# Performance work log

Measured on AMD Instinct MI355X. Metric: run time of the kernel, lower is better.

The kernel has to match this reference:

```python
import jax, jax.numpy as jnp
import numpy as np

B, N, K = 16, 512, 30
H = 128
NHEADS = 4
NLAYERS = 3
VOCAB = 20
NUM_RBF = 16
NUM_POS = 16
NEG_INF = jnp.float32(np.finfo(np.float32).min)


def _ln(x, eps=1e-6):
    m = jnp.mean(x, -1, keepdims=True)
    v = jnp.var(x, -1, keepdims=True)
    return (x - m) / jnp.sqrt(v + eps)


def _gather_nodes(nodes, E_idx):
    # nodes [B,N,C], E_idx [B,N,K] -> [B,N,K,C]
    return jax.vmap(lambda n, idx: n[idx])(nodes, E_idx)


def _normalize(x):
    return x / (jnp.linalg.norm(x, axis=-1, keepdims=True) + 1e-7)


def _dihedrals(X):
    b, n = X.shape[0], X.shape[1]
    Xb = X[:, :, :3, :].reshape(b, 3 * n, 3)  # N, CA, C atoms flattened
    dX = Xb[:, 1:] - Xb[:, :-1]
    U = _normalize(dX)
    u2, u1, u0 = U[:, :-2], U[:, 1:-1], U[:, 2:]
    n2 = _normalize(jnp.cross(u2, u1))
    n1 = _normalize(jnp.cross(u1, u0))
    cosD = jnp.clip(jnp.sum(n2 * n1, -1), -1.0 + 1e-7, 1.0 - 1e-7)
    Dang = jnp.sign(jnp.sum(u2 * n1, -1)) * jnp.arccos(cosD)
    Dang = jnp.pad(Dang, ((0, 0), (1, 2)))
    Dang = Dang.reshape(b, n, 3)
    return jnp.concatenate([jnp.cos(Dang), jnp.sin(Dang)], -1)  # [B,N,6]


def _features(X, mask, Wfn, bfn, Wfe, bfe):
    X_ca = X[:, :, 1, :]
    mask2d = mask[:, :, None] * mask[:, None, :]
    dX = X_ca[:, :, None, :] - X_ca[:, None, :, :]
    D = mask2d * jnp.sqrt(jnp.sum(dX * dX, -1) + 1e-6)  # [B,N,N]
    D_max = jnp.max(D, -1, keepdims=True)
    D_adjust = D + (1.0 - mask2d) * D_max
    negD, E_idx = jax.lax.top_k(-D_adjust, K)  # K nearest neighbors
    D_neighbors = -negD
    mu = jnp.linspace(0.0, 20.0, NUM_RBF)
    sigma = 20.0 / NUM_RBF
    rbf = jnp.exp(-(((D_neighbors[..., None] - mu) / sigma) ** 2))  # [B,N,K,16]
    ii = jnp.arange(N)[None, :, None]
    d = (E_idx - ii)[..., None].astype(jnp.float32)
    freq = jnp.exp(jnp.arange(0, NUM_POS, 2, dtype=jnp.float32) * (-np.log(10000.0) / NUM_POS))
    ang = d * freq
    epos = jnp.concatenate([jnp.cos(ang), jnp.sin(ang)], -1)  # [B,N,K,16]
    E = jnp.concatenate([epos, rbf], -1)  # [B,N,K,32]
    V = _dihedrals(X)
    V = _ln(V @ Wfn + bfn)
    E = _ln(E @ Wfe + bfe)
    return V, E, E_idx


def _attn(hV, hE, WQ, WK, WV, WO, mask_attend=None):
    b, n, h = hV.shape
    k = hE.shape[2]
    d = h // NHEADS
    Q = (hV @ WQ).reshape(b, n, NHEADS, d)
    Kt = (hE @ WK).reshape(b, n, k, NHEADS, d)
    Vt = (hE @ WV).reshape(b, n, k, NHEADS, d)
    logits = jnp.einsum('bnhd,bnkhd->bnhk', Q, Kt) / np.sqrt(d).astype(np.float32)
    if mask_attend is not None:
        m = mask_attend[:, :, None, :]
        logits = jnp.where(m > 0, logits, NEG_INF)
        attend = jax.nn.softmax(logits, -1) * m
    else:
        attend = jax.nn.softmax(logits, -1)
    out = jnp.einsum('bnhk,bnkhd->bnhd', attend, Vt).reshape(b, n, h)
    return out @ WO


def _layer(hV, hEV, WQ, WK, WV, WO, W1, b1, W2, b2, mask_V=None, mask_attend=None):
    dh = _attn(hV, hEV, WQ, WK, WV, WO, mask_attend)
    hV = _ln(hV + dh)
    dh = jax.nn.relu(hV @ W1 + b1) @ W2 + b2
    hV = _ln(hV + dh)
    if mask_V is not None:
        hV = mask_V[..., None] * hV
    return hV


def _forward(X, mask, S, Wfn, bfn, Wfe, bfe, Wv, bv, We, be, Ws,
             enc_WQ, enc_WK, enc_WV, enc_WO, enc_W1, enc_b1, enc_W2, enc_b2,
             dec_WQ, dec_WK, dec_WV, dec_WO, dec_W1, dec_b1, dec_W2, dec_b2,
             W_out, b_out):
    V, E, E_idx = _features(X, mask, Wfn, bfn, Wfe, bfe)
    h_V = V @ Wv + bv
    h_E = E @ We + be
    # encoder attention mask
    mask_nb = _gather_nodes(mask[..., None], E_idx)[..., 0]
    mask_attend_enc = mask[:, :, None] * mask_nb
    for l in range(NLAYERS):
        h_EV = jnp.concatenate([h_E, _gather_nodes(h_V, E_idx)], -1)
        h_V = _layer(h_V, h_EV, enc_WQ[l], enc_WK[l], enc_WV[l], enc_WO[l],
                     enc_W1[l], enc_b1[l], enc_W2[l], enc_b2[l],
                     mask_V=mask, mask_attend=mask_attend_enc)
    # decoder: identity permutation -> rank == position, ar mask = E_idx < i
    ar = (E_idx < jnp.arange(N)[None, :, None]).astype(h_V.dtype)
    mask_attend = ar[..., None]  # [B,N,K,1]
    h_S = Ws[S]
    h_ES = jnp.concatenate([h_E, _gather_nodes(h_S, E_idx)], -1)
    h_ES_enc = jnp.concatenate([h_E, jnp.zeros_like(h_E[..., :H])], -1)
    h_ESV_enc = jnp.concatenate([h_ES_enc, _gather_nodes(h_V, E_idx)], -1)
    mask_1D = mask[:, :, None, None]
    mask_bw = mask_1D * mask_attend
    mask_fw = mask_1D * (1.0 - mask_attend)
    h_fw = mask_fw * h_ESV_enc
    for l in range(NLAYERS):
        h_ESV = jnp.concatenate([h_ES, _gather_nodes(h_V, E_idx)], -1)
        h_ESV = mask_bw * h_ESV + h_fw
        h_V = _layer(h_V, h_ESV, dec_WQ[l], dec_WK[l], dec_WV[l], dec_WO[l],
                     dec_W1[l], dec_b1[l], dec_W2[l], dec_b2[l], mask_V=mask)
    logits = h_V @ W_out + b_out
    return jax.nn.log_softmax(logits, -1)


def setup_inputs():
    key = jax.random.key(0)
    ks = iter(jax.random.split(key, 80))

    def lin(i, o):
        return jax.random.normal(next(ks), (i, o), dtype=jnp.float32) * (1.0 / np.sqrt(i)).astype(np.float32)

    def stack(i, o):
        return jnp.stack([lin(i, o) for _ in range(NLAYERS)])

    inp = {}
    inp['X'] = jax.random.normal(next(ks), (B, N, 4, 3), dtype=jnp.float32) * 3.0
    inp['mask'] = jnp.ones((B, N), jnp.float32)
    inp['S'] = jax.random.randint(next(ks), (B, N), 0, VOCAB)
    inp['Wfn'] = lin(6, H); inp['bfn'] = jnp.zeros((H,), jnp.float32)
    inp['Wfe'] = lin(NUM_POS + NUM_RBF, H); inp['bfe'] = jnp.zeros((H,), jnp.float32)
    inp['Wv'] = lin(H, H); inp['bv'] = jnp.zeros((H,), jnp.float32)
    inp['We'] = lin(H, H); inp['be'] = jnp.zeros((H,), jnp.float32)
    inp['Ws'] = jax.random.normal(next(ks), (VOCAB, H), dtype=jnp.float32) * 0.1
    inp['enc_WQ'] = stack(H, H); inp['enc_WK'] = stack(2 * H, H)
    inp['enc_WV'] = stack(2 * H, H); inp['enc_WO'] = stack(H, H)
    inp['enc_W1'] = stack(H, 4 * H); inp['enc_b1'] = jnp.zeros((NLAYERS, 4 * H), jnp.float32)
    inp['enc_W2'] = stack(4 * H, H); inp['enc_b2'] = jnp.zeros((NLAYERS, H), jnp.float32)
    inp['dec_WQ'] = stack(H, H); inp['dec_WK'] = stack(3 * H, H)
    inp['dec_WV'] = stack(3 * H, H); inp['dec_WO'] = stack(H, H)
    inp['dec_W1'] = stack(H, 4 * H); inp['dec_b1'] = jnp.zeros((NLAYERS, 4 * H), jnp.float32)
    inp['dec_W2'] = stack(4 * H, H); inp['dec_b2'] = jnp.zeros((NLAYERS, H), jnp.float32)
    inp['W_out'] = lin(H, VOCAB); inp['b_out'] = jnp.zeros((VOCAB,), jnp.float32)
    return inp


def reference(X, mask, S, Wfn, bfn, Wfe, bfe, Wv, bv, We, be, Ws,
              enc_WQ, enc_WK, enc_WV, enc_WO, enc_W1, enc_b1, enc_W2, enc_b2,
              dec_WQ, dec_WK, dec_WV, dec_WO, dec_W1, dec_b1, dec_W2, dec_b2,
              W_out, b_out):
    return _forward(X, mask, S, Wfn, bfn, Wfe, bfe, Wv, bv, We, be, Ws,
                    enc_WQ, enc_WK, enc_WV, enc_WO, enc_W1, enc_b1, enc_W2, enc_b2,
                    dec_WQ, dec_WK, dec_WV, dec_WO, dec_W1, dec_b1, dec_W2, dec_b2,
                    W_out, b_out)
```

## Files before the change

### kernel.cpp

```cpp
#include <hip/hip_runtime.h>
#include <hip/hip_bf16.h>
#include <math.h>

#define DEVFN __device__ __forceinline__

constexpr int B_ = 16, N_ = 512, K_ = 30, H_ = 128;
constexpr int NH_ = 4, V_ = 20;
constexpr int BN_ = B_ * N_;
constexpr float NEG_INF_ = -3.4028235e38f;
constexpr int FRAG_ = H_ * H_;
constexpr int FRAG2_ = H_ * 4 * H_;

typedef unsigned short ushort_t;
using short8 = __attribute__((ext_vector_type(8))) short;
using f32x4  = __attribute__((ext_vector_type(4))) float;

DEVFN ushort_t bf16rn(float x) {
  unsigned u = __float_as_uint(x);
  return (ushort_t)((u + 0x7fffu + ((u >> 16) & 1u)) >> 16);
}
DEVFN float bf16tof(ushort_t h) { return __uint_as_float(((unsigned)h) << 16); }

__global__ __launch_bounds__(256) void topk_kernel(const float* __restrict__ X,
    const float* __restrict__ mask, int* __restrict__ E_idx, float* __restrict__ Dnb) {
  __shared__ float xs[N_ * 3];
  __shared__ float ds[N_];
  __shared__ float fred[4];
  __shared__ unsigned long long kred[4];
  int b = blockIdx.x / N_, i = blockIdx.x % N_;
  int t = threadIdx.x;
  for (int j = t; j < N_; j += 256) {
    const float* p = X + ((size_t)(b * N_ + j) * 4 + 1) * 3;
    xs[j * 3 + 0] = p[0]; xs[j * 3 + 1] = p[1]; xs[j * 3 + 2] = p[2];
  }
  __syncthreads();
  float xi0 = xs[i * 3], xi1 = xs[i * 3 + 1], xi2 = xs[i * 3 + 2];
  float mi = mask[b * N_ + i];
  float lmax = -3.4e38f;
  for (int j = t; j < N_; j += 256) {
    float dx = __fsub_rn(xi0, xs[j * 3]);
    float dy = __fsub_rn(xi1, xs[j * 3 + 1]);
    float dz = __fsub_rn(xi2, xs[j * 3 + 2]);
    float m2 = __fmul_rn(mi, mask[b * N_ + j]);
    float s = __fadd_rn(__fadd_rn(__fadd_rn(__fmul_rn(dx, dx), __fmul_rn(dy, dy)),
                                  __fmul_rn(dz, dz)), 1e-6f);
    float D = __fmul_rn(m2, __fsqrt_rn(s));
    ds[j] = D;
    lmax = fmaxf(lmax, D);
  }
  #pragma unroll
  for (int off = 32; off > 0; off >>= 1) lmax = fmaxf(lmax, __shfl_xor(lmax, off, 64));
  if ((t & 63) == 0) fred[t >> 6] = lmax;
  __syncthreads();
  float Dmax = fmaxf(fmaxf(fred[0], fred[1]), fmaxf(fred[2], fred[3]));
  for (int j = t; j < N_; j += 256) {
    float m2 = __fmul_rn(mi, mask[b * N_ + j]);
    ds[j] = __fadd_rn(ds[j], __fmul_rn(__fsub_rn(1.f, m2), Dmax));
  }
  __syncthreads();
  for (int kk = 0; kk < K_; kk++) {
    unsigned long long best = ~0ull;
    for (int j = t; j < N_; j += 256) {
      unsigned long long key = (((unsigned long long)__float_as_uint(ds[j])) << 32)
                             | (unsigned)(N_ - 1 - j);
      if (key < best) best = key;
    }
    #pragma unroll
    for (int off = 32; off > 0; off >>= 1) {
      unsigned long long o = __shfl_xor(best, off, 64);
      if (o < best) best = o;
    }
    if ((t & 63) == 0) kred[t >> 6] = best;
    __syncthreads();
    if (t == 0) {
      unsigned long long k0 = kred[0];
      #pragma unroll
      for (int q = 1; q < 4; q++) if (kred[q] < k0) k0 = kred[q];
      int j = N_ - 1 - (int)(k0 & 0xffffffffull);
      E_idx[blockIdx.x * K_ + kk] = j;
      Dnb[blockIdx.x * K_ + kk] = __uint_as_float((unsigned)(k0 >> 32));
      ds[j] = 3.4028235e38f;
    }
    __syncthreads();
  }
}

DEVFN void load_atom(const float* X, int b, int m, float* p) {
  const float* q = X + ((size_t)(b * N_ + m / 3) * 4 + (m % 3)) * 3;
  p[0] = q[0]; p[1] = q[1]; p[2] = q[2];
}
DEVFN void cross3(const float* a, const float* b, float* c) {
  c[0] = a[1] * b[2] - a[2] * b[1];
  c[1] = a[2] * b[0] - a[0] * b[2];
  c[2] = a[0] * b[1] - a[1] * b[0];
}
DEVFN void norm3(float* v) {
  float n = sqrtf(v[0] * v[0] + v[1] * v[1] + v[2] * v[2]) + 1e-7f;
  v[0] /= n; v[1] /= n; v[2] /= n;
}
__global__ __launch_bounds__(256) void dihedral_kernel(const float* __restrict__ X, float* __restrict__ Vf) {
  int idx = blockIdx.x * blockDim.x + threadIdx.x;
  if (idx >= BN_) return;
  int b = idx / N_, n = idx % N_;
  float cs[3], sn[3];
  for (int s = 0; s < 3; s++) {
    int p = 3 * n + s;
    float a = 0.f;
    if (p >= 1 && p <= 3 * N_ - 3) {
      int tt = p - 1;
      float u[3][3], prev[3], cur[3];
      load_atom(X, b, tt, prev);
      for (int q = 0; q < 3; q++) {
        load_atom(X, b, tt + q + 1, cur);
        float d0 = cur[0] - prev[0], d1 = cur[1] - prev[1], d2 = cur[2] - prev[2];
        float nr = sqrtf(d0 * d0 + d1 * d1 + d2 * d2) + 1e-7f;
        u[q][0] = d0 / nr; u[q][1] = d1 / nr; u[q][2] = d2 / nr;
        prev[0] = cur[0]; prev[1] = cur[1]; prev[2] = cur[2];
      }
      float n2v[3], n1v[3];
      cross3(u[0], u[1], n2v); norm3(n2v);
      cross3(u[1], u[2], n1v); norm3(n1v);
      float cd = n2v[0] * n1v[0] + n2v[1] * n1v[1] + n2v[2] * n1v[2];
      cd = fminf(fmaxf(cd, -1.f + 1e-7f), 1.f - 1e-7f);
      float dt = u[0][0] * n1v[0] + u[0][1] * n1v[1] + u[0][2] * n1v[2];
      float sg = (dt > 0.f) ? 1.f : ((dt < 0.f) ? -1.f : 0.f);
      a = sg * acosf(cd);
    }
    cs[s] = cosf(a); sn[s] = sinf(a);
  }
  float* o = Vf + (size_t)idx * 6;
  o[0] = cs[0]; o[1] = cs[1]; o[2] = cs[2]; o[3] = sn[0]; o[4] = sn[1]; o[5] = sn[2];
}

__global__ __launch_bounds__(H_) void node_embed_kernel(const float* __restrict__ Vf,
    const float* __restrict__ Wfn, const float* __restrict__ bfn,
    const float* __restrict__ Wv, const float* __restrict__ bv, float* __restrict__ hV) {
  int node = blockIdx.x, t = threadIdx.x;
  const int w = t >> 6, l = t & 63;
  __shared__ float v6[6];
  __shared__ __attribute__((aligned(16))) float t1[H_];
  __shared__ float wred[2];
  if (t < 6) v6[t] = Vf[(size_t)node * 6 + t];
  __syncthreads();
  float acc = bfn[t];
  for (int f = 0; f < 6; f++) acc = fmaf(v6[f], Wfn[f * H_ + t], acc);
  float s1 = acc;
  #pragma unroll
  for (int off = 32; off > 0; off >>= 1) s1 += __shfl_xor(s1, off, 64);
  if (l == 0) wred[w] = s1;
  __syncthreads();
  float mean = (wred[0] + wred[1]) * (1.f / H_);
  float d0 = acc - mean;
  float s2 = d0 * d0;
  #pragma unroll
  for (int off = 32; off > 0; off >>= 1) s2 += __shfl_xor(s2, off, 64);
  __syncthreads();
  if (l == 0) wred[w] = s2;
  __syncthreads();
  float var = (wred[0] + wred[1]) * (1.f / H_);
  t1[t] = d0 * rsqrtf(var + 1e-6f);
  __syncthreads();
  float o = bv[t];
  for (int j4 = 0; j4 < H_ / 4; j4++) {
    float4 xv = ((const float4*)t1)[j4];
    int j = j4 * 4;
    o = fmaf(xv.x, Wv[(j + 0) * H_ + t],
        fmaf(xv.y, Wv[(j + 1) * H_ + t],
        fmaf(xv.z, Wv[(j + 2) * H_ + t],
        fmaf(xv.w, Wv[(j + 3) * H_ + t], o))));
  }
  hV[(size_t)node * H_ + t] = o;
}

__global__ __launch_bounds__(256) void prep_edge_w_kernel(const float* __restrict__ Wfe,
    const float* __restrict__ We, ushort_t* __restrict__ feHi, ushort_t* __restrict__ feLo,
    ushort_t* __restrict__ weHi, ushort_t* __restrict__ weLo) {
  if (blockIdx.x == 0) {
    for (int i = 0; i < 4096 / 256; i++) {
      int lin = i * 256 + threadIdx.x;
      int k = lin >> 7, c = lin & 127;
      float x = Wfe[lin];
      int gk = k >> 3, j = k & 7;
      int nt = c >> 4, cc = c & 15;
      int oidx = (nt * 64 + gk * 16 + cc) * 8 + j;
      ushort_t hb = bf16rn(x);
      feHi[oidx] = hb;
      feLo[oidx] = bf16rn(x - bf16tof(hb));
    }
  } else {
    for (int i = 0; i < FRAG_ / 256; i++) {
      int lin = i * 256 + threadIdx.x;
      int k = lin >> 7, c = lin & 127;
      float x = We[lin];
      int ks = k >> 5, gk = (k >> 3) & 3, j = k & 7;
      int nt = c >> 4, cc = c & 15;
      int oidx = ((ks * 8 + nt) * 64 + gk * 16 + cc) * 8 + j;
      ushort_t hb = bf16rn(x);
      weHi[oidx] = hb;
      weLo[oidx] = bf16rn(x - bf16tof(hb));
    }
  }
}

__global__ __launch_bounds__(256) void prep_wkt_kernel(const float* __restrict__ eWK,
    const float* __restrict__ dWK, float* __restrict__ outT) {
  int m = blockIdx.x;
  const float* W = (m < 3) ? (eWK + (size_t)m * 2 * H_ * H_)
                           : (dWK + (size_t)(m - 3) * 3 * H_ * H_);
  float* o = outT + (size_t)m * FRAG_;
  for (int i = 0; i < FRAG_ / 256; i++) {
    int lin = i * 256 + threadIdx.x;
    int c = lin >> 7, f = lin & 127;
    o[lin] = W[f * H_ + c];
  }
}

constexpr int EEB_ = 32;
constexpr int FPS_ = 40;
__global__ __launch_bounds__(128) void edge_embed_kernel(const int* __restrict__ E_idx,
    const float* __restrict__ Dnb,
    const ushort_t* __restrict__ feHi, const ushort_t* __restrict__ feLo,
    const float* __restrict__ bfe,
    const ushort_t* __restrict__ weHi, const ushort_t* __restrict__ weLo,
    const float* __restrict__ be, float* __restrict__ hE) {
  int e0 = blockIdx.x * EEB_, t = threadIdx.x;
  const int w = t >> 6, l = t & 63, c0 = l & 15, g = l >> 4;
  __shared__ ushort_t fhi[EEB_ * FPS_], flo[EEB_ * FPS_];
  __shared__ __attribute__((aligned(16))) char sbuf[EEB_ * H_ * 4];
  float* buf = (float*)sbuf;
  ushort_t* p2hi = (ushort_t*)sbuf;
  ushort_t* p2lo = (ushort_t*)(sbuf + EEB_ * H_ * 2);
  __shared__ float mst[EEB_], ist[EEB_];

  #pragma unroll
  for (int it = 0; it < 8; it++) {
    int id = it * 128 + t;
    int r = id >> 5, f = id & 31;
    int e = e0 + r;
    int n = (e / K_) % N_;
    float v;
    if (f < 16) {
      int jj = (f < 8) ? f : (f - 8);
      float freq = expf(-logf(10000.f) * (2.f * jj) / 16.f);
      float ang = (float)(E_idx[e] - n) * freq;
      v = (f < 8) ? cosf(ang) : sinf(ang);
    } else {
      int rr = f - 16;
      float mu = 20.f * (float)rr / 15.f;
      float z = (Dnb[e] - mu) * (1.f / 1.25f);
      v = expf(-z * z);
    }
    ushort_t hb = bf16rn(v);
    fhi[r * FPS_ + f] = hb;
    flo[r * FPS_ + f] = bf16rn(v - bf16tof(hb));
  }
  __syncthreads();

  {
    short8 ah[2], al[2];
    #pragma unroll
    for (int mt = 0; mt < 2; mt++) {
      int r = mt * 16 + c0;
      ah[mt] = *(const short8*)&fhi[r * FPS_ + g * 8];
      al[mt] = *(const short8*)&flo[r * FPS_ + g * 8];
    }
    #pragma unroll
    for (int nt = 0; nt < 4; nt++) {
      int ntg = w * 4 + nt;
      size_t boff = (size_t)((ntg * 64 + l) * 8);
      short8 bh = *(const short8*)(feHi + boff);
      short8 bl = *(const short8*)(feLo + boff);
      int c = ntg * 16 + c0;
      float bb = bfe[c];
      #pragma unroll
      for (int mt = 0; mt < 2; mt++) {
        f32x4 a = f32x4{0.f, 0.f, 0.f, 0.f};
        a = __builtin_amdgcn_mfma_f32_16x16x32_bf16(ah[mt], bh, a, 0, 0, 0);
        a = __builtin_amdgcn_mfma_f32_16x16x32_bf16(al[mt], bh, a, 0, 0, 0);
        a = __builtin_amdgcn_mfma_f32_16x16x32_bf16(ah[mt], bl, a, 0, 0, 0);
        a = __builtin_amdgcn_mfma_f32_16x16x32_bf16(al[mt], bl, a, 0, 0, 0);
        #pragma unroll
        for (int j = 0; j < 4; j++) {
          int row = mt * 16 + g * 4 + j;
          buf[row * H_ + c] = a[j] + bb;
        }
      }
    }
  }
  __syncthreads();

  {
    int row = t >> 2, li = t & 3;
    float s = 0.f;
    for (int i = 0; i < 32; i++) {
      int col = li + 4 * ((i + row) & 31);
      s += buf[row * H_ + col];
    }
    s += __shfl_xor(s, 1, 64); s += __shfl_xor(s, 2, 64);
    float mean = s * (1.f / H_);
    float vs = 0.f;
    for (int i = 0; i < 32; i++) {
      int col = li + 4 * ((i + row) & 31);
      float d = buf[row * H_ + col] - mean;
      vs = fmaf(d, d, vs);
    }
    vs += __shfl_xor(vs, 1, 64); vs += __shfl_xor(vs, 2, 64);
    if (li == 0) { mst[row] = mean; ist[row] = rsqrtf(vs * (1.f / H_) + 1e-6f); }
  }
  __syncthreads();

  float vreg[32];
  #pragma unroll
  for (int it = 0; it < 4; it++) {
    int id = it * 128 + t;
    int r = id >> 4, u = id & 15;
    float mean = mst[r], inv = ist[r];
    #pragma unroll
    for (int e2 = 0; e2 < 8; e2++) vreg[it * 8 + e2] = (buf[r * H_ + u * 8 + e2] - mean) * inv;
  }
  __syncthreads();
  #pragma unroll
  for (int it = 0; it < 4; it++) {
    int id = it * 128 + t;
    int r = id >> 4, u = id & 15;
    short8 h8, l8;
    #pragma unroll
    for (int e2 = 0; e2 < 8; e2++) {
      float x = vreg[it * 8 + e2];
      ushort_t hb = bf16rn(x);
      h8[e2] = (short)hb;
      l8[e2] = (short)bf16rn(x - bf16tof(hb));
    }
    int us = u ^ (r & 15);
    *(short8*)&p2hi[r * 128 + us * 8] = h8;
    *(short8*)&p2lo[r * 128 + us * 8] = l8;
  }
  __syncthreads();

  short8 ah2[2][4], al2[2][4];
  #pragma unroll
  for (int mt = 0; mt < 2; mt++) {
    int r = mt * 16 + c0;
    #pragma unroll
    for (int ks = 0; ks < 4; ks++) {
      int us = (ks * 4 + g) ^ c0;
      ah2[mt][ks] = *(const short8*)&p2hi[r * 128 + us * 8];
      al2[mt][ks] = *(const short8*)&p2lo[r * 128 + us * 8];
    }
  }
  f32x4 acc2[2][4];
  #pragma unroll
  for (int mt = 0; mt < 2; mt++)
    #pragma unroll
    for (int nt = 0; nt < 4; nt++) acc2[mt][nt] = f32x4{0.f, 0.f, 0.f, 0.f};
  #pragma unroll
  for (int ks = 0; ks < 4; ks++) {
    #pragma unroll
    for (int nt = 0; nt < 4; nt++) {
      int ntg = w * 4 + nt;
      size_t boff = (size_t)(((ks * 8 + ntg) * 64 + l) * 8);
      short8 bh = *(const short8*)(weHi + boff);
      short8 bl = *(const short8*)(weLo + boff);
      #pragma unroll
      for (int mt = 0; mt < 2; mt++) {
        acc2[mt][nt] = __builtin_amdgcn_mfma_f32_16x16x32_bf16(ah2[mt][ks], bh, acc2[mt][nt], 0, 0, 0);
        acc2[mt][nt] = __builtin_amdgcn_mfma_f32_16x16x32_bf16(al2[mt][ks], bh, acc2[mt][nt], 0, 0, 0);
        acc2[mt][nt] = __builtin_amdgcn_mfma_f32_16x16x32_bf16(ah2[mt][ks], bl, acc2[mt][nt], 0, 0, 0);
        acc2[mt][nt] = __builtin_amdgcn_mfma_f32_16x16x32_bf16(al2[mt][ks], bl, acc2[mt][nt], 0, 0, 0);
      }
    }
  }
  #pragma unroll
  for (int mt = 0; mt < 2; mt++) {
    #pragma unroll
    for (int nt = 0; nt < 4; nt++) {
      int c = (w * 4 + nt) * 16 + c0;
      float bb = be[c];
      #pragma unroll
      for (int j = 0; j < 4; j++) {
        int row = mt * 16 + g * 4 + j;
        hE[(size_t)(e0 + row) * H_ + c] = acc2[mt][nt][j] + bb;
      }
    }
  }
}

__global__ __launch_bounds__(128) void node_proj_kernel(const float* __restrict__ x1,
    const float* __restrict__ Wa1, const float* __restrict__ Wb1,
    float* __restrict__ oa, float* __restrict__ ob) {
  constexpr int NT = 16;
  int n0 = blockIdx.x * NT, t = threadIdx.x;
  __shared__ __attribute__((aligned(16))) float xs1[NT * H_];
  #pragma unroll
  for (int u = 0; u < NT; u++) xs1[u * H_ + t] = x1[(size_t)(n0 + u) * H_ + t];
  __syncthreads();
  float aa[NT], ab[NT];
  #pragma unroll
  for (int u = 0; u < NT; u++) { aa[u] = 0.f; ab[u] = 0.f; }
  for (int j4 = 0; j4 < H_ / 4; j4++) {
    int j = j4 * 4;
    float wa0 = Wa1[(j + 0) * H_ + t], wa1 = Wa1[(j + 1) * H_ + t];
    float wa2 = Wa1[(j + 2) * H_ + t], wa3 = Wa1[(j + 3) * H_ + t];
    float wb0 = Wb1[(j + 0) * H_ + t], wb1 = Wb1[(j + 1) * H_ + t];
    float wb2 = Wb1[(j + 2) * H_ + t], wb3 = Wb1[(j + 3) * H_ + t];
    #pragma unroll
    for (int u = 0; u < NT; u++) {
      float4 xv = ((const float4*)(xs1 + u * H_))[j4];
      aa[u] = fmaf(xv.x, wa0, fmaf(xv.y, wa1, fmaf(xv.z, wa2, fmaf(xv.w, wa3, aa[u]))));
      ab[u] = fmaf(xv.x, wb0, fmaf(xv.y, wb1, fmaf(xv.z, wb2, fmaf(xv.w, wb3, ab[u]))));
    }
  }
  #pragma unroll
  for (int u = 0; u < NT; u++) {
    oa[(size_t)(n0 + u) * H_ + t] = aa[u];
    ob[(size_t)(n0 + u) * H_ + t] = ab[u];
  }
}

__global__ __launch_bounds__(128) void node_proj3_kernel(const int* __restrict__ S,
    const float* __restrict__ Ws, const float* __restrict__ din, const float* __restrict__ henc,
    const float* __restrict__ WK2, const float* __restrict__ WV2,
    const float* __restrict__ WK3, const float* __restrict__ WV3,
    float* __restrict__ nKb, float* __restrict__ nVb,
    float* __restrict__ nKe, float* __restrict__ nVe) {
  constexpr int NT = 8;
  int n0 = blockIdx.x * NT, t = threadIdx.x;
  __shared__ __attribute__((aligned(16))) float xs1[NT * H_];
  __shared__ __attribute__((aligned(16))) float xs2[NT * H_];
  __shared__ __attribute__((aligned(16))) float xs3[NT * H_];
  #pragma unroll
  for (int u = 0; u < NT; u++) {
    int node = n0 + u;
    xs1[u * H_ + t] = Ws[(size_t)S[node] * H_ + t];
    xs2[u * H_ + t] = din[(size_t)node * H_ + t];
    xs3[u * H_ + t] = henc[(size_t)node * H_ + t];
  }
  __syncthreads();
  float aKb[NT], aVb[NT], aKe[NT], aVe[NT];
  #pragma unroll
  for (int u = 0; u < NT; u++) { aKb[u] = 0.f; aVb[u] = 0.f; aKe[u] = 0.f; aVe[u] = 0.f; }
  for (int j4 = 0; j4 < H_ / 4; j4++) {
    int j = j4 * 4;
    float k20 = WK2[(j + 0) * H_ + t], k21 = WK2[(j + 1) * H_ + t];
    float k22 = WK2[(j + 2) * H_ + t], k23 = WK2[(j + 3) * H_ + t];
    float v20 = WV2[(j + 0) * H_ + t], v21 = WV2[(j + 1) * H_ + t];
    float v22 = WV2[(j + 2) * H_ + t], v23 = WV2[(j + 3) * H_ + t];
    float k30 = WK3[(j + 0) * H_ + t], k31 = WK3[(j + 1) * H_ + t];
    float k32 = WK3[(j + 2) * H_ + t], k33 = WK3[(j + 3) * H_ + t];
    float v30 = WV3[(j + 0) * H_ + t], v31 = WV3[(j + 1) * H_ + t];
    float v32 = WV3[(j + 2) * H_ + t], v33 = WV3[(j + 3) * H_ + t];
    #pragma unroll
    for (int u = 0; u < NT; u++) {
      float4 a = ((const float4*)(xs1 + u * H_))[j4];
      float4 b = ((const float4*)(xs2 + u * H_))[j4];
      float4 c = ((const float4*)(xs3 + u * H_))[j4];
      aKb[u] = fmaf(a.x, k20, fmaf(a.y, k21, fmaf(a.z, k22, fmaf(a.w, k23, aKb[u]))));
      aKb[u] = fmaf(b.x, k30, fmaf(b.y, k31, fmaf(b.z, k32, fmaf(b.w, k33, aKb[u]))));
      aVb[u] = fmaf(a.x, v20, fmaf(a.y, v21, fmaf(a.z, v22, fmaf(a.w, v23, aVb[u]))));
      aVb[u] = fmaf(b.x, v30, fmaf(b.y, v31, fmaf(b.z, v32, fmaf(b.w, v33, aVb[u]))));
      aKe[u] = fmaf(c.x, k30, fmaf(c.y, k31, fmaf(c.z, k32, fmaf(c.w, k33, aKe[u]))));
      aVe[u] = fmaf(c.x, v30, fmaf(c.y, v31, fmaf(c.z, v32, fmaf(c.w, v33, aVe[u]))));
    }
  }
  #pragma unroll
  for (int u = 0; u < NT; u++) {
    size_t g = (size_t)(n0 + u) * H_ + t;
    nKb[g] = aKb[u]; nVb[g] = aVb[u]; nKe[g] = aKe[u]; nVe[g] = aVe[u];
  }
}

__global__ __launch_bounds__(256) void prep_wfrag2_kernel(const float* __restrict__ eW1,
    const float* __restrict__ eW2, const float* __restrict__ dW1, const float* __restrict__ dW2,
    ushort_t* __restrict__ hiOut, ushort_t* __restrict__ loOut) {
  int m = blockIdx.x;
  const float* W; int C;
  if (m < 3)      { W = eW1 + (size_t)m * FRAG2_;       C = 4 * H_; }
  else if (m < 6) { W = eW2 + (size_t)(m - 3) * FRAG2_; C = H_; }
  else if (m < 9) { W = dW1 + (size_t)(m - 6) * FRAG2_; C = 4 * H_; }
  else            { W = dW2 + (size_t)(m - 9) * FRAG2_; C = H_; }
  ushort_t* hi = hiOut + (size_t)m * FRAG2_;
  ushort_t* lo = loOut + (size_t)m * FRAG2_;
  int ntn = C >> 4;
  int cshift = (C == 512) ? 9 : 7;
  for (int i = 0; i < FRAG2_ / 256; i++) {
    int lin = i * 256 + threadIdx.x;
    int k = lin >> cshift, c = lin & (C - 1);
    float x = W[lin];
    int ks = k >> 5, gk = (k >> 3) & 3, j = k & 7;
    int nt = c >> 4, cc = c & 15;
    int lane = gk * 16 + cc;
    int oidx = ((ks * ntn + nt) * 64 + lane) * 8 + j;
    ushort_t hb = bf16rn(x);
    hi[oidx] = hb;
    lo[oidx] = bf16rn(x - bf16tof(hb));
  }
}

template<bool ENC>
__global__ __launch_bounds__(128) void attn_kernel(const float* __restrict__ hV_in,
    const float* __restrict__ hE, const int* __restrict__ E_idx, const float* __restrict__ mask,
    const float* __restrict__ WQ, const float* __restrict__ WK1T, const float* __restrict__ WV1,
    const float* __restrict__ WO,
    const float* __restrict__ nKb, const float* __restrict__ nVb,
    const float* __restrict__ nKe, const float* __restrict__ nVe,
    float* __restrict__ hV_out) {
  const int node = blockIdx.x;
  const int b = node / N_, n = node % N_;
  const int t = threadIdx.x;
  const int w = t >> 6, l = t & 63;
  const int head = t >> 5, lane32 = t & 31;

  __shared__ __attribute__((aligned(16))) float heb[K_ * H_];
  __shared__ float x0s[H_];
  __shared__ float qs[H_];
  __shared__ float qa[4][H_ + 4];
  __shared__ float ob[H_];
  __shared__ float scb[NH_ * 32];
  __shared__ int nbs[K_];
  __shared__ float wred[2];

  x0s[t] = hV_in[(size_t)node * H_ + t];
  if (t < K_) nbs[t] = E_idx[node * K_ + t];
  {
    const float4* src = (const float4*)(hE + (size_t)node * (K_ * H_));
    float4* dst = (float4*)heb;
    #pragma unroll
    for (int i = 0; i < (K_ * H_ / 4) / 128 + 1; i++) {
      int id = i * 128 + t;
      if (id < K_ * H_ / 4) dst[id] = src[id];
    }
  }
  if ((t & 31) >= K_) scb[t] = NEG_INF_;
  __syncthreads();

  float qreg = 0.f;
  for (int j4 = 0; j4 < H_ / 4; j4++) {
    float4 xv = ((const float4*)x0s)[j4];
    int j = j4 * 4;
    qreg = fmaf(xv.x, WQ[(j + 0) * H_ + t],
           fmaf(xv.y, WQ[(j + 1) * H_ + t],
           fmaf(xv.z, WQ[(j + 2) * H_ + t],
           fmaf(xv.w, WQ[(j + 3) * H_ + t], qreg))));
  }
  qs[t] = qreg;
  float mi = mask[b * N_ + n];
  __syncthreads();

  {
    float a0 = 0.f, a1 = 0.f, a2 = 0.f, a3 = 0.f;
    #pragma unroll 4
    for (int c = 0; c < 32; c++) {
      a0 = fmaf(WK1T[(c      ) * H_ + t], qs[c      ], a0);
      a1 = fmaf(WK1T[(c + 32 ) * H_ + t], qs[c + 32 ], a1);
      a2 = fmaf(WK1T[(c + 64 ) * H_ + t], qs[c + 64 ], a2);
      a3 = fmaf(WK1T[(c + 96 ) * H_ + t], qs[c + 96 ], a3);
    }
    qa[0][t] = a0; qa[1][t] = a1; qa[2][t] = a2; qa[3][t] = a3;
  }
  __syncthreads();

  const float qk0 = qa[head][lane32],      qk1 = qa[head][lane32 + 32];
  const float qk2 = qa[head][lane32 + 64], qk3 = qa[head][lane32 + 96];
  constexpr int KT = 10;
  const float scale = 0.17677669529663687f;
  for (int kt = 0; kt < K_; kt += KT) {
    float gb[KT], ge[KT], gm[KT];
    #pragma unroll
    for (int u = 0; u < KT; u++) {
      int nb = nbs[kt + u];
      size_t nbg = (size_t)(b * N_ + nb) * H_ + t;
      gb[u] = nKb[nbg];
      if (!ENC) ge[u] = nKe[nbg];
      else      gm[u] = mask[b * N_ + nb];
    }
    #pragma unroll
    for (int u = 0; u < KT; u++) {
      int k = kt + u;
      int nb = nbs[k];
      const float* he = heb + k * H_;
      float ep = fmaf(qk0, he[lane32],
                 fmaf(qk1, he[lane32 + 32],
                 fmaf(qk2, he[lane32 + 64], qk3 * he[lane32 + 96])));
      float prod;
      if (ENC) {
        prod = fmaf(qreg, gb[u], ep);
      } else {
        float ar = (nb < n) ? 1.f : 0.f;
        float bw = mi * ar, fw = mi * (1.f - ar);
        float nodek = fmaf(bw, gb[u], fw * ge[u]);
        prod = fmaf(mi, ep, qreg * nodek);
      }
      #pragma unroll
      for (int off = 16; off > 0; off >>= 1) prod += __shfl_xor(prod, off, 32);
      if (lane32 == 0) {
        if (ENC) {
          float m2 = mi * gm[u];
          scb[head * 32 + k] = (m2 > 0.f) ? prod * scale : NEG_INF_;
        } else {
          scb[head * 32 + k] = prod * scale;
        }
      }
    }
  }
  __syncthreads();

  {
    float s = scb[t];
    float mx = s;
    #pragma unroll
    for (int off = 16; off > 0; off >>= 1) mx = fmaxf(mx, __shfl_xor(mx, off, 32));
    float ev = expf(s - mx);
    float sum = ev;
    #pragma unroll
    for (int off = 16; off > 0; off >>= 1) sum += __shfl_xor(sum, off, 32);
    scb[t] = ev / sum;
  }
  __syncthreads();

  {
    float a0 = 0.f, a1 = 0.f, a2 = 0.f, a3 = 0.f;
    #pragma unroll
    for (int k = 0; k < K_; k++) {
      float hv = heb[k * H_ + t];
      a0 = fmaf(scb[0 * 32 + k], hv, a0);
      a1 = fmaf(scb[1 * 32 + k], hv, a1);
      a2 = fmaf(scb[2 * 32 + k], hv, a2);
      a3 = fmaf(scb[3 * 32 + k], hv, a3);
    }
    qa[0][t] = a0; qa[1][t] = a1; qa[2][t] = a2; qa[3][t] = a3;
  }
  float onode = 0.f;
  for (int kt = 0; kt < K_; kt += KT) {
    float gv[KT], gve[KT];
    #pragma unroll
    for (int u = 0; u < KT; u++) {
      int nb = nbs[kt + u];
      size_t nbg = (size_t)(b * N_ + nb) * H_ + t;
      gv[u] = nVb[nbg];
      if (!ENC) gve[u] = nVe[nbg];
    }
    #pragma unroll
    for (int u = 0; u < KT; u++) {
      int k = kt + u;
      float att = scb[head * 32 + k];
      if (ENC) {
        onode = fmaf(att, gv[u], onode);
      } else {
        int nb = nbs[k];
        float ar = (nb < n) ? 1.f : 0.f;
        float bw = mi * ar, fw = mi * (1.f - ar);
        onode = fmaf(att, fmaf(bw, gv[u], fw * gve[u]), onode);
      }
    }
  }
  __syncthreads();

  float oe = 0.f;
  {
    const float* agh = qa[head];
    #pragma unroll 4
    for (int f = 0; f < H_; f++) oe = fmaf(agh[f], WV1[f * H_ + t], oe);
  }
  float o = ENC ? (oe + onode) : fmaf(mi, oe, onode);
  ob[t] = o; __syncthreads();

  float dh = 0.f;
  for (int j4 = 0; j4 < H_ / 4; j4++) {
    float4 ov = ((const float4*)ob)[j4];
    int j = j4 * 4;
    dh = fmaf(ov.x, WO[(j + 0) * H_ + t],
         fmaf(ov.y, WO[(j + 1) * H_ + t],
         fmaf(ov.z, WO[(j + 2) * H_ + t],
         fmaf(ov.w, WO[(j + 3) * H_ + t], dh))));
  }
  float r = x0s[t] + dh;
  float s1 = r;
  #pragma unroll
  for (int off = 32; off > 0; off >>= 1) s1 += __shfl_xor(s1, off, 64);
  if (l == 0) wred[w] = s1;
  __syncthreads();
  float mean = (wred[0] + wred[1]) * (1.f / H_);
  float d0 = r - mean;
  float s2 = d0 * d0;
  #pragma unroll
  for (int off = 32; off > 0; off >>= 1) s2 += __shfl_xor(s2, off, 64);
  __syncthreads();
  if (l == 0) wred[w] = s2;
  __syncthreads();
  float var = (wred[0] + wred[1]) * (1.f / H_);
  hV_out[(size_t)node * H_ + t] = d0 * rsqrtf(var + 1e-6f);
}

constexpr int NTF_ = 8;
__global__ __launch_bounds__(128) void ffn_kernel(float* __restrict__ hV, const float* __restrict__ mask,
    const ushort_t* __restrict__ w1hi, const ushort_t* __restrict__ w1lo,
    const ushort_t* __restrict__ w2hi, const ushort_t* __restrict__ w2lo,
    const float* __restrict__ b1, const float* __restrict__ b2) {
  int n0 = blockIdx.x * NTF_, t = threadIdx.x;
  const int w = t >> 6, l = t & 63, c0 = l & 15, g = l >> 4;
  __shared__ __attribute__((aligned(16))) ushort_t xhi[16 * H_], xlo[16 * H_];
  __shared__ __attribute__((aligned(16))) ushort_t hpl[2][2 * 16 * H_];
  __shared__ float mst[16], ist[16];
  float* obuf = (float*)&hpl[0][0];

  #pragma unroll
  for (int it = 0; it < 2; it++) {
    int id = it * 128 + t;
    int r = id >> 4, u = id & 15;
    short8 h8 = {0,0,0,0,0,0,0,0}, l8 = {0,0,0,0,0,0,0,0};
    if (r < NTF_) {
      const float4* p = (const float4*)(hV + (size_t)(n0 + r) * H_ + u * 8);
      float4 f0 = p[0], f1 = p[1];
      float xv[8] = {f0.x, f0.y, f0.z, f0.w, f1.x, f1.y, f1.z, f1.w};
      #pragma unroll
      for (int e = 0; e < 8; e++) {
        ushort_t hb = bf16rn(xv[e]);
        h8[e] = (short)hb;
        l8[e] = (short)bf16rn(xv[e] - bf16tof(hb));
      }
    }
    int us = u ^ (r & 15);
    *(short8*)&xhi[r * 128 + us * 8] = h8;
    *(short8*)&xlo[r * 128 + us * 8] = l8;
  }
  __syncthreads();

  short8 axh[4], axl[4];
  #pragma unroll
  for (int ks = 0; ks < 4; ks++) {
    int us = ((ks * 4 + g) ^ c0) * 8;
    axh[ks] = *(const short8*)&xhi[c0 * 128 + us];
    axl[ks] = *(const short8*)&xlo[c0 * 128 + us];
  }

  ushort_t* myhhi = &hpl[w][0];
  ushort_t* myhlo = &hpl[w][16 * H_];
  f32x4 accO[8];
  #pragma unroll
  for (int nt = 0; nt < 8; nt++) accO[nt] = f32x4{0.f, 0.f, 0.f, 0.f};

  #pragma unroll
  for (int cc = 0; cc < 2; cc++) {
    int c = 2 * w + cc;
    f32x4 a1[8];
    #pragma unroll
    for (int nt = 0; nt < 8; nt++) a1[nt] = f32x4{0.f, 0.f, 0.f, 0.f};
    #pragma unroll
    for (int ks = 0; ks < 4; ks++) {
      #pragma unroll
      for (int nt = 0; nt < 8; nt++) {
        size_t boff = (size_t)(((ks * 32 + (c * 8 + nt)) * 64 + l) * 8);
        short8 bh = *(const short8*)(w1hi + boff);
        short8 bl = *(const short8*)(w1lo + boff);
        a1[nt] = __builtin_amdgcn_mfma_f32_16x16x32_bf16(axh[ks], bh, a1[nt], 0, 0, 0);
        a1[nt] = __builtin_amdgcn_mfma_f32_16x16x32_bf16(axl[ks], bh, a1[nt], 0, 0, 0);
        a1[nt] = __builtin_amdgcn_mfma_f32_16x16x32_bf16(axh[ks], bl, a1[nt], 0, 0, 0);
        a1[nt] = __builtin_amdgcn_mfma_f32_16x16x32_bf16(axl[ks], bl, a1[nt], 0, 0, 0);
      }
    }
    #pragma unroll
    for (int nt = 0; nt < 8; nt++) {
      int col = nt * 16 + c0;
      float bb = b1[c * 128 + col];
      #pragma unroll
      for (int j = 0; j < 4; j++) {
        int row = g * 4 + j;
        float hv = fmaxf(a1[nt][j] + bb, 0.f);
        ushort_t hb = bf16rn(hv);
        ushort_t lb = bf16rn(hv - bf16tof(hb));
        int us2 = ((col >> 3) ^ row) * 8 + (col & 7);
        myhhi[row * 128 + us2] = hb;
        myhlo[row * 128 + us2] = lb;
      }
    }
    #pragma unroll
    for (int ks = 0; ks < 4; ks++) {
      int us2 = ((ks * 4 + g) ^ c0) * 8;
      short8 ahh = *(const short8*)&myhhi[c0 * 128 + us2];
      short8 ahl = *(const short8*)&myhlo[c0 * 128 + us2];
      #pragma unroll
      for (int nt = 0; nt < 8; nt++) {
        size_t boff = (size_t)((((c * 4 + ks) * 8 + nt) * 64 + l) * 8);
        short8 bh = *(const short8*)(w2hi + boff);
        short8 bl = *(const short8*)(w2lo + boff);
        accO[nt] = __builtin_amdgcn_mfma_f32_16x16x32_bf16(ahh, bh, accO[nt], 0, 0, 0);
        accO[nt] = __builtin_amdgcn_mfma_f32_16x16x32_bf16(ahl, bh, accO[nt], 0, 0, 0);
        accO[nt] = __builtin_amdgcn_mfma_f32_16x16x32_bf16(ahh, bl, accO[nt], 0, 0, 0);
        accO[nt] = __builtin_amdgcn_mfma_f32_16x16x32_bf16(ahl, bl, accO[nt], 0, 0, 0);
      }
    }
  }

  if (w == 0) {
    #pragma unroll
    for (int nt = 0; nt < 8; nt++) {
      #pragma unroll
      for (int j = 0; j < 4; j++) {
        int row = g * 4 + j;
        if (row < NTF_) obuf[row * H_ + nt * 16 + c0] = accO[nt][j];
      }
    }
  }
  __syncthreads();
  if (w == 1) {
    #pragma unroll
    for (int nt = 0; nt < 8; nt++) {
      #pragma unroll
      for (int j = 0; j < 4; j++) {
        int row = g * 4 + j;
        if (row < NTF_) obuf[row * H_ + nt * 16 + c0] += accO[nt][j];
      }
    }
  }
  __syncthreads();

  float rv[NTF_];
  {
    int un = t >> 3, e = t & 7;
    float bb = b2[t];
    #pragma unroll
    for (int u = 0; u < NTF_; u++) {
      int us = (un ^ u) * 8 + e;
      float xr = bf16tof(xhi[u * 128 + us]) + bf16tof(xlo[u * 128 + us]);
      rv[u] = xr + obuf[u * H_ + t] + bb;
    }
  }
  #pragma unroll
  for (int u = 0; u < NTF_; u++) obuf[u * H_ + t] = rv[u];
  __syncthreads();
  {
    int row = t >> 3, li = t & 7;
    float s = 0.f;
    if (row < NTF_) {
      for (int i = 0; i < 16; i++) s += obuf[row * H_ + li + 8 * i];
    }
    s += __shfl_xor(s, 1, 64); s += __shfl_xor(s, 2, 64); s += __shfl_xor(s, 4, 64);
    float mean = s * (1.f / H_);
    float vs = 0.f;
    if (row < NTF_) {
      for (int i = 0; i < 16; i++) {
        float d = obuf[row * H_ + li + 8 * i] - mean;
        vs = fmaf(d, d, vs);
      }
    }
    vs += __shfl_xor(vs, 1, 64); vs += __shfl_xor(vs, 2, 64); vs += __shfl_xor(vs, 4, 64);
    if (li == 0 && row < NTF_) { mst[row] = mean; ist[row] = rsqrtf(vs * (1.f / H_) + 1e-6f); }
  }
  __syncthreads();
  #pragma unroll
  for (int u = 0; u < NTF_; u++) {
    float y = (rv[u] - mst[u]) * ist[u] * mask[n0 + u];
    hV[(size_t)(n0 + u) * H_ + t] = y;
  }
}

__global__ __launch_bounds__(128) void out_kernel(const float* __restrict__ hV,
    const float* __restrict__ Wout, const float* __restrict__ bout, float* __restrict__ out) {
  int g = threadIdx.x >> 6, t = threadIdx.x & 63;
  int node = blockIdx.x * 2 + g;
  __shared__ float x[2][H_];
  __shared__ float lg[2][V_];
  __shared__ float lse[2];
  x[g][t] = hV[(size_t)node * H_ + t];
  x[g][t + 64] = hV[(size_t)node * H_ + t + 64];
  __syncthreads();
  if (t < V_) {
    float a = bout[t];
    for (int h = 0; h < H_; h++) a = fmaf(x[g][h], Wout[h * V_ + t], a);
    lg[g][t] = a;
  }
  __syncthreads();
  if (t == 0) {
    float mx = -3.4e38f;
    for (int v = 0; v < V_; v++) mx = fmaxf(mx, lg[g][v]);
    float s = 0.f;
    for (int v = 0; v < V_; v++) s += expf(lg[g][v] - mx);
    lse[g] = mx + logf(s);
  }
  __syncthreads();
  if (t < V_) out[(size_t)node * V_ + t] = lg[g][t] - lse[g];
}

extern "C" void kernel_launch(void* const* d_in, const int* in_sizes, int n_in,
                              void* d_out, int out_size, void* d_ws, size_t ws_size,
                              hipStream_t stream) {
  const float* X    = (const float*)d_in[0];
  const float* mask = (const float*)d_in[1];
  const int*   S    = (const int*)d_in[2];
  const float* Wfn  = (const float*)d_in[3];
  const float* bfn  = (const float*)d_in[4];
  const float* Wfe  = (const float*)d_in[5];
  const float* bfe  = (const float*)d_in[6];
  const float* Wv   = (const float*)d_in[7];
  const float* bv   = (const float*)d_in[8];
  const float* We   = (const float*)d_in[9];
  const float* be   = (const float*)d_in[10];
  const float* Ws   = (const float*)d_in[11];
  const float* eWQ  = (const float*)d_in[12];
  const float* eWK  = (const float*)d_in[13];
  const float* eWV  = (const float*)d_in[14];
  const float* eWO  = (const float*)d_in[15];
  const float* eW1  = (const float*)d_in[16];
  const float* eb1  = (const float*)d_in[17];
  const float* eW2  = (const float*)d_in[18];
  const float* eb2  = (const float*)d_in[19];
  const float* dWQ  = (const float*)d_in[20];
  const float* dWK  = (const float*)d_in[21];
  const float* dWV  = (const float*)d_in[22];
  const float* dWO  = (const float*)d_in[23];
  const float* dW1  = (const float*)d_in[24];
  const float* db1  = (const float*)d_in[25];
  const float* dW2  = (const float*)d_in[26];
  const float* db2  = (const float*)d_in[27];
  const float* Wout = (const float*)d_in[28];
  const float* bout = (const float*)d_in[29];
  float* out = (float*)d_out;

  char* w = (char*)d_ws;
  int*    eidx = (int*)w;     w += (size_t)BN_ * K_ * 4;
  float*  dnb  = (float*)w;   w += (size_t)BN_ * K_ * 4;
  float*  vf   = (float*)w;   w += (size_t)BN_ * 6 * 4;
  float*  hVa  = (float*)w;   w += (size_t)BN_ * H_ * 4;
  float*  hVb  = (float*)w;   w += (size_t)BN_ * H_ * 4;
  float*  hVc  = (float*)w;   w += (size_t)BN_ * H_ * 4;
  float*  nKb  = (float*)w;   w += (size_t)BN_ * H_ * 4;
  float*  nVb  = (float*)w;   w += (size_t)BN_ * H_ * 4;
  float*  nKe  = (float*)w;   w += (size_t)BN_ * H_ * 4;
  float*  nVe  = (float*)w;   w += (size_t)BN_ * H_ * 4;
  float*  hE   = (float*)w;   w += (size_t)BN_ * K_ * H_ * 4;
  float*  wkt  = (float*)w;   w += (size_t)6 * FRAG_ * 4;
  ushort_t* wf2Hi = (ushort_t*)w; w += (size_t)12 * FRAG2_ * 2;
  ushort_t* wf2Lo = (ushort_t*)w; w += (size_t)12 * FRAG2_ * 2;
  ushort_t* feHi = (ushort_t*)w; w += (size_t)4096 * 2;
  ushort_t* feLo = (ushort_t*)w; w += (size_t)4096 * 2;
  ushort_t* weHi = (ushort_t*)w; w += (size_t)FRAG_ * 2;
  ushort_t* weLo = (ushort_t*)w; w += (size_t)FRAG_ * 2;

  topk_kernel<<<BN_, 256, 0, stream>>>(X, mask, eidx, dnb);
  dihedral_kernel<<<(BN_ + 255) / 256, 256, 0, stream>>>(X, vf);
  node_embed_kernel<<<BN_, H_, 0, stream>>>(vf, Wfn, bfn, Wv, bv, hVa);
  prep_edge_w_kernel<<<2, 256, 0, stream>>>(Wfe, We, feHi, feLo, weHi, weLo);
  edge_embed_kernel<<<BN_ * K_ / EEB_, 128, 0, stream>>>(eidx, dnb, feHi, feLo, bfe, weHi, weLo, be, hE);
  prep_wkt_kernel<<<6, 256, 0, stream>>>(eWK, dWK, wkt);
  prep_wfrag2_kernel<<<12, 256, 0, stream>>>(eW1, eW2, dW1, dW2, wf2Hi, wf2Lo);

  float* cur = hVa; float* nxt = hVb;
  for (int l = 0; l < 3; l++) {
    const float* WK = eWK + (size_t)l * 2 * H_ * H_;
    const float* WV = eWV + (size_t)l * 2 * H_ * H_;
    node_proj_kernel<<<BN_ / 16, H_, 0, stream>>>(cur,
        WK + (size_t)H_ * H_, WV + (size_t)H_ * H_, nKb, nVb);
    attn_kernel<true><<<BN_, H_, 0, stream>>>(cur, hE, eidx, mask,
        eWQ + (size_t)l * H_ * H_,
        wkt + (size_t)l * FRAG_,
        WV,
        eWO + (size_t)l * H_ * H_,
        nKb, nVb, nullptr, nullptr, nxt);
    ffn_kernel<<<BN_ / NTF_, 128, 0, stream>>>(nxt, mask,
        wf2Hi + (size_t)l * FRAG2_, wf2Lo + (size_t)l * FRAG2_,
        wf2Hi + (size_t)(3 + l) * FRAG2_, wf2Lo + (size_t)(3 + l) * FRAG2_,
        eb1 + (size_t)l * 4 * H_, eb2 + (size_t)l * H_);
    float* tmp = cur; cur = nxt; nxt = tmp;
  }
  float* henc = cur;
  float* din = henc;
  float* douts[3] = { hVa, hVc, hVa };
  for (int l = 0; l < 3; l++) {
    const float* WK = dWK + (size_t)l * 3 * H_ * H_;
    const float* WV = dWV + (size_t)l * 3 * H_ * H_;
    node_proj3_kernel<<<BN_ / 8, H_, 0, stream>>>(S, Ws, din, henc,
        WK + (size_t)H_ * H_, WV + (size_t)H_ * H_,
        WK + (size_t)2 * H_ * H_, WV + (size_t)2 * H_ * H_,
        nKb, nVb, nKe, nVe);
    attn_kernel<false><<<BN_, H_, 0, stream>>>(din, hE, eidx, mask,
        dWQ + (size_t)l * H_ * H_,
        wkt + (size_t)(3 + l) * FRAG_,
        WV,
        dWO + (size_t)l * H_ * H_,
        nKb, nVb, nKe, nVe, douts[l]);
    ffn_kernel<<<BN_ / NTF_, 128, 0, stream>>>(douts[l], mask,
        wf2Hi + (size_t)(6 + l) * FRAG2_, wf2Lo + (size_t)(6 + l) * FRAG2_,
        wf2Hi + (size_t)(9 + l) * FRAG2_, wf2Lo + (size_t)(9 + l) * FRAG2_,
        db1 + (size_t)l * 4 * H_, db2 + (size_t)l * H_);
    din = douts[l];
  }
  out_kernel<<<BN_ / 2, 128, 0, stream>>>(din, Wout, bout, out);
}
```

Measured before the change: 1.731 ms.

## Restructure top-k kernel to one wavefront per query with register-resident keys

The top-k neighbor kernel now handles four query residues per block, one per 64-wide wavefront. Each lane keeps its 8 candidate distance keys in registers. Each of the 30 selection rounds is a wavefront shuffle reduction, and only the winning lane recomputes its local minimum. This removes the block-wide __syncthreads and shared-memory rescans from every round and cuts the number of blocks and coordinate loads by a factor of four. In exchange it uses more registers for the 64-bit keys, and the masked max is now taken per wavefront within one query, which matches the reference semantics.

```diff
diff --git a/kernel.cpp b/kernel.cpp
--- a/kernel.cpp
+++ b/kernel.cpp
@@ -21,67 +21,73 @@
 }
 DEVFN float bf16tof(ushort_t h) { return __uint_as_float(((unsigned)h) << 16); }
 
+constexpr int TQ_ = 4;
 __global__ __launch_bounds__(256) void topk_kernel(const float* __restrict__ X,
     const float* __restrict__ mask, int* __restrict__ E_idx, float* __restrict__ Dnb) {
   __shared__ float xs[N_ * 3];
-  __shared__ float ds[N_];
-  __shared__ float fred[4];
-  __shared__ unsigned long long kred[4];
-  int b = blockIdx.x / N_, i = blockIdx.x % N_;
+  __shared__ float ms[N_];
+  int blk = blockIdx.x;
+  int b = blk / (N_ / TQ_);
+  int i0 = (blk % (N_ / TQ_)) * TQ_;
   int t = threadIdx.x;
+  int wv = t >> 6, l = t & 63;
   for (int j = t; j < N_; j += 256) {
     const float* p = X + ((size_t)(b * N_ + j) * 4 + 1) * 3;
     xs[j * 3 + 0] = p[0]; xs[j * 3 + 1] = p[1]; xs[j * 3 + 2] = p[2];
-  }
-  __syncthreads();
-  float xi0 = xs[i * 3], xi1 = xs[i * 3 + 1], xi2 = xs[i * 3 + 2];
-  float mi = mask[b * N_ + i];
+    ms[j] = mask[b * N_ + j];
+  }
+  __syncthreads();
+  const int i = i0 + wv;
+  const float xi0 = xs[i * 3], xi1 = xs[i * 3 + 1], xi2 = xs[i * 3 + 2];
+  const float mi = ms[i];
+  float D[8];
   float lmax = -3.4e38f;
-  for (int j = t; j < N_; j += 256) {
+  #pragma unroll
+  for (int e = 0; e < 8; e++) {
+    int j = l * 8 + e;
     float dx = __fsub_rn(xi0, xs[j * 3]);
     float dy = __fsub_rn(xi1, xs[j * 3 + 1]);
     float dz = __fsub_rn(xi2, xs[j * 3 + 2]);
-    float m2 = __fmul_rn(mi, mask[b * N_ + j]);
+    float m2 = __fmul_rn(mi, ms[j]);
     float s = __fadd_rn(__fadd_rn(__fadd_rn(__fmul_rn(dx, dx), __fmul_rn(dy, dy)),
                                   __fmul_rn(dz, dz)), 1e-6f);
-    float D = __fmul_rn(m2, __fsqrt_rn(s));
-    ds[j] = D;
-    lmax = fmaxf(lmax, D);
+    float Dv = __fmul_rn(m2, __fsqrt_rn(s));
+    D[e] = Dv;
+    lmax = fmaxf(lmax, Dv);
   }
   #pragma unroll
   for (int off = 32; off > 0; off >>= 1) lmax = fmaxf(lmax, __shfl_xor(lmax, off, 64));
-  if ((t & 63) == 0) fred[t >> 6] = lmax;
-  __syncthreads();
-  float Dmax = fmaxf(fmaxf(fred[0], fred[1]), fmaxf(fred[2], fred[3]));
-  for (int j = t; j < N_; j += 256) {
-    float m2 = __fmul_rn(mi, mask[b * N_ + j]);
-    ds[j] = __fadd_rn(ds[j], __fmul_rn(__fsub_rn(1.f, m2), Dmax));
-  }
-  __syncthreads();
+  unsigned long long key[8];
+  unsigned long long lmin = ~0ull;
+  #pragma unroll
+  for (int e = 0; e < 8; e++) {
+    int j = l * 8 + e;
+    float m2 = __fmul_rn(mi, ms[j]);
+    float d = __fadd_rn(D[e], __fmul_rn(__fsub_rn(1.f, m2), lmax));
+    unsigned long long k = (((unsigned long long)__float_as_uint(d)) << 32)
+                         | (unsigned)(N_ - 1 - j);
+    key[e] = k;
+    if (k < lmin) lmin = k;
+  }
   for (int kk = 0; kk < K_; kk++) {
-    unsigned long long best = ~0ull;
-    for (int j = t; j < N_; j += 256) {
-      unsigned long long key = (((unsigned long long)__float_as_uint(ds[j])) << 32)
-                             | (unsigned)(N_ - 1 - j);
-      if (key < best) best = key;
-    }
+    unsigned long long m = lmin;
     #pragma unroll
     for (int off = 32; off > 0; off >>= 1) {
-      unsigned long long o = __shfl_xor(best, off, 64);
-      if (o < best) best = o;
-    }
-    if ((t & 63) == 0) kred[t >> 6] = best;
-    __syncthreads();
-    if (t == 0) {
-      unsigned long long k0 = kred[0];
-      #pragma unroll
-      for (int q = 1; q < 4; q++) if (kred[q] < k0) k0 = kred[q];
-      int j = N_ - 1 - (int)(k0 & 0xffffffffull);
-      E_idx[blockIdx.x * K_ + kk] = j;
-      Dnb[blockIdx.x * K_ + kk] = __uint_as_float((unsigned)(k0 >> 32));
-      ds[j] = 3.4028235e38f;
-    }
-    __syncthreads();
+      unsigned long long o = __shfl_xor(m, off, 64);
+      if (o < m) m = o;
+    }
+    int j = N_ - 1 - (int)(m & 0xffffffffull);
+    if (l == 0) {
+      E_idx[(size_t)(b * N_ + i) * K_ + kk] = j;
+      Dnb[(size_t)(b * N_ + i) * K_ + kk] = __uint_as_float((unsigned)(m >> 32));
+    }
+    if ((j >> 3) == l) {
+      key[j & 7] = ~0ull;
+      unsigned long long nm = key[0];
+      #pragma unroll
+      for (int e = 1; e < 8; e++) if (key[e] < nm) nm = key[e];
+      lmin = nm;
+    }
   }
 }
 
@@ -936,7 +942,7 @@
   ushort_t* weHi = (ushort_t*)w; w += (size_t)FRAG_ * 2;
   ushort_t* weLo = (ushort_t*)w; w += (size_t)FRAG_ * 2;
 
-  topk_kernel<<<BN_, 256, 0, stream>>>(X, mask, eidx, dnb);
+  topk_kernel<<<BN_ / TQ_, 256, 0, stream>>>(X, mask, eidx, dnb);
   dihedral_kernel<<<(BN_ + 255) / 256, 256, 0, stream>>>(X, vf);
   node_embed_kernel<<<BN_, H_, 0, stream>>>(vf, Wfn, bfn, Wv, bv, hVa);
   prep_edge_w_kernel<<<2, 256, 0, stream>>>(Wfe, We, feHi, feLo, weHi, weLo);
```

Result: faster. 1.632 ms (median of 2 runs) (-5.7%).
